# Kernel tuning notes

Measured on AMD Instinct MI355X. Metric: run time of the kernel, lower is better.

Reference implementation:

```python
import jax, jax.numpy as jnp
import numpy as np

B, T, VOCAB = 8192, 1024, 10000

def setup_inputs() -> dict:
    key = jax.random.key(0)
    k1, k2, k3, k4 = jax.random.split(key, 4)
    sample_seq = jax.random.randint(k1, (B, T), 0, VOCAB, dtype=jnp.int32)
    sample_seqLogprobs = jax.random.normal(k2, (B, T), dtype=jnp.float32)
    sample_value = jax.random.normal(k3, (B, T), dtype=jnp.float32)
    sample_reward = jax.random.normal(k4, (B, T), dtype=jnp.float32)
    return {
        "sample_seq": sample_seq,
        "sample_seqLogprobs": sample_seqLogprobs,
        "sample_value": sample_value,
        "sample_reward": sample_reward,
    }

def reference(sample_seq, sample_seqLogprobs, sample_value, sample_reward):
    # Vectorized version of the per-element python loop: zero out every token
    # at or after the first EOS (token id 0). cumsum>0 of the EOS indicator is
    # the running-max (cummax) of (seq==0).
    at_or_after_eos = jnp.cumsum((sample_seq == 0).astype(jnp.int32), axis=1) > 0
    seq = jnp.where(at_or_after_eos, 0, sample_seq)  # [B, T]

    # mask = (seq>0), shifted right by one with a leading column of ones
    mask = (seq > 0).astype(sample_seqLogprobs.dtype)
    mask = jnp.concatenate(
        [jnp.ones((mask.shape[0], 1), mask.dtype), mask[:, :-1]], axis=1
    )

    # sample_reward is a detached numpy array in the original (no grad)
    reward = jax.lax.stop_gradient(sample_reward)
    reward_diff = reward - sample_value  # [B, T]

    # masked REINFORCE loss, normalized by number of valid tokens
    output = -sample_seqLogprobs * reward_diff * mask
    loss = output.sum() / mask.sum()
    return loss
```

## Files before the change

### kernel.cpp

```cpp
#include <hip/hip_runtime.h>

#define BROWS 8192
#define TLEN  1024

__global__ __launch_bounds__(256) void row_reduce_kernel(
    const int*   __restrict__ seq,
    const float* __restrict__ logp,
    const float* __restrict__ value,
    const float* __restrict__ reward,
    double*      __restrict__ row_sum,
    double*      __restrict__ row_cnt)
{
    const int row  = blockIdx.x * 4 + (threadIdx.x >> 6);
    const int lane = threadIdx.x & 63;

    const size_t rowoff = (size_t)row * TLEN;
    const int4*   s4 = (const int4*)  (seq    + rowoff);
    const float4* l4 = (const float4*)(logp   + rowoff);
    const float4* v4 = (const float4*)(value  + rowoff);
    const float4* r4 = (const float4*)(reward + rowoff);

    int4   s[4];
    float4 l[4], v[4], r[4];
    #pragma unroll
    for (int k = 0; k < 4; ++k) {
        const int idx = k * 64 + lane;
        s[k] = s4[idx];
        l[k] = l4[idx];
        v[k] = v4[idx];
        r[k] = r4[idx];
    }

    int fz = TLEN;
    #pragma unroll
    for (int k = 3; k >= 0; --k) {
        const int base = k * 256 + lane * 4;
        if (s[k].w == 0) fz = base + 3;
        if (s[k].z == 0) fz = base + 2;
        if (s[k].y == 0) fz = base + 1;
        if (s[k].x == 0) fz = base + 0;
    }

    #pragma unroll
    for (int off = 32; off > 0; off >>= 1)
        fz = min(fz, __shfl_xor(fz, off, 64));

    double acc = 0.0;
    #pragma unroll
    for (int k = 0; k < 4; ++k) {
        const int base = k * 256 + lane * 4;
        if (base + 0 <= fz) acc += (double)(-l[k].x * (r[k].x - v[k].x));
        if (base + 1 <= fz) acc += (double)(-l[k].y * (r[k].y - v[k].y));
        if (base + 2 <= fz) acc += (double)(-l[k].z * (r[k].z - v[k].z));
        if (base + 3 <= fz) acc += (double)(-l[k].w * (r[k].w - v[k].w));
    }

    #pragma unroll
    for (int off = 32; off > 0; off >>= 1)
        acc += __shfl_xor(acc, off, 64);

    if (lane == 0) {
        row_sum[row] = acc;
        row_cnt[row] = (double)min(fz + 1, TLEN);
    }
}

__global__ __launch_bounds__(256) void final_reduce_kernel(
    const double* __restrict__ row_sum,
    const double* __restrict__ row_cnt,
    float*        __restrict__ out)
{
    const int tid  = threadIdx.x;
    const int lane = tid & 63;
    const int wave = tid >> 6;

    double s = 0.0, c = 0.0;
    for (int i = tid; i < BROWS; i += 256) {
        s += row_sum[i];
        c += row_cnt[i];
    }
    #pragma unroll
    for (int off = 32; off > 0; off >>= 1) {
        s += __shfl_xor(s, off, 64);
        c += __shfl_xor(c, off, 64);
    }
    __shared__ double ls[4], lc[4];
    if (lane == 0) { ls[wave] = s; lc[wave] = c; }
    __syncthreads();
    if (tid == 0) {
        double ts = ls[0] + ls[1] + ls[2] + ls[3];
        double tc = lc[0] + lc[1] + lc[2] + lc[3];
        out[0] = (float)(ts / tc);
    }
}

extern "C" void kernel_launch(void* const* d_in, const int* in_sizes, int n_in,
                              void* d_out, int out_size, void* d_ws, size_t ws_size,
                              hipStream_t stream) {
    const int*   seq    = (const int*)  d_in[0];
    const float* logp   = (const float*)d_in[1];
    const float* value  = (const float*)d_in[2];
    const float* reward = (const float*)d_in[3];
    float* out = (float*)d_out;

    double* row_sum = (double*)d_ws;
    double* row_cnt = row_sum + BROWS;

    row_reduce_kernel<<<BROWS / 4, 256, 0, stream>>>(seq, logp, value, reward,
                                                     row_sum, row_cnt);
    final_reduce_kernel<<<1, 256, 0, stream>>>(row_sum, row_cnt, out);
}
```

Baseline: 156.5 us.

## Split EOS-position scan and masked sum into separate kernels

The fused row kernel is split in two. The first kernel finds the first-EOS index per row and writes it out. The second kernel reads logprob, value and reward with one full row per 256-thread block, covering four strided rows, and sums per block; the final kernel derives the token count from the stored indices. This shrinks the per-row dependency so the float loads are not tied to the sequence scan, but it adds an extra kernel launch and serialises the two passes over memory.

Result: no change. 156.0 us (-0.3%).

```diff
diff --git a/kernel.cpp b/kernel.cpp
--- a/kernel.cpp
+++ b/kernel.cpp
@@ -2,34 +2,21 @@
 
 #define BROWS 8192
 #define TLEN  1024
+#define NBLK  2048
+#define RPB   4
 
-__global__ __launch_bounds__(256) void row_reduce_kernel(
-    const int*   __restrict__ seq,
-    const float* __restrict__ logp,
-    const float* __restrict__ value,
-    const float* __restrict__ reward,
-    double*      __restrict__ row_sum,
-    double*      __restrict__ row_cnt)
+__global__ __launch_bounds__(256) void fz_kernel(
+    const int* __restrict__ seq,
+    int*       __restrict__ fz_out)
 {
     const int row  = blockIdx.x * 4 + (threadIdx.x >> 6);
     const int lane = threadIdx.x & 63;
 
-    const size_t rowoff = (size_t)row * TLEN;
-    const int4*   s4 = (const int4*)  (seq    + rowoff);
-    const float4* l4 = (const float4*)(logp   + rowoff);
-    const float4* v4 = (const float4*)(value  + rowoff);
-    const float4* r4 = (const float4*)(reward + rowoff);
-
-    int4   s[4];
-    float4 l[4], v[4], r[4];
+    const int4* s4 = (const int4*)(seq + (size_t)row * TLEN);
+    int4 s[4];
     #pragma unroll
-    for (int k = 0; k < 4; ++k) {
-        const int idx = k * 64 + lane;
-        s[k] = s4[idx];
-        l[k] = l4[idx];
-        v[k] = v4[idx];
-        r[k] = r4[idx];
-    }
+    for (int k = 0; k < 4; ++k)
+        s[k] = s4[k * 64 + lane];
 
     int fz = TLEN;
     #pragma unroll
@@ -40,34 +27,58 @@
         if (s[k].y == 0) fz = base + 1;
         if (s[k].x == 0) fz = base + 0;
     }
-
     #pragma unroll
     for (int off = 32; off > 0; off >>= 1)
         fz = min(fz, __shfl_xor(fz, off, 64));
 
+    if (lane == 0) fz_out[row] = fz;
+}
+
+__global__ __launch_bounds__(256) void sum_kernel(
+    const float* __restrict__ logp,
+    const float* __restrict__ value,
+    const float* __restrict__ reward,
+    const int*   __restrict__ fz_in,
+    double*      __restrict__ blk_sum)
+{
+    const int tid = threadIdx.x;
+
+    float4 l[RPB], v[RPB], r[RPB];
+    int    fz[RPB];
+    #pragma unroll
+    for (int k = 0; k < RPB; ++k) {
+        const int    row = blockIdx.x + k * NBLK;
+        const size_t off = (size_t)row * TLEN;
+        l[k]  = ((const float4*)(logp   + off))[tid];
+        v[k]  = ((const float4*)(value  + off))[tid];
+        r[k]  = ((const float4*)(reward + off))[tid];
+        fz[k] = fz_in[row];
+    }
+
+    const int t0 = tid * 4;
     double acc = 0.0;
     #pragma unroll
-    for (int k = 0; k < 4; ++k) {
-        const int base = k * 256 + lane * 4;
-        if (base + 0 <= fz) acc += (double)(-l[k].x * (r[k].x - v[k].x));
-        if (base + 1 <= fz) acc += (double)(-l[k].y * (r[k].y - v[k].y));
-        if (base + 2 <= fz) acc += (double)(-l[k].z * (r[k].z - v[k].z));
-        if (base + 3 <= fz) acc += (double)(-l[k].w * (r[k].w - v[k].w));
+    for (int k = 0; k < RPB; ++k) {
+        if (t0 + 0 <= fz[k]) acc += (double)(-l[k].x * (r[k].x - v[k].x));
+        if (t0 + 1 <= fz[k]) acc += (double)(-l[k].y * (r[k].y - v[k].y));
+        if (t0 + 2 <= fz[k]) acc += (double)(-l[k].z * (r[k].z - v[k].z));
+        if (t0 + 3 <= fz[k]) acc += (double)(-l[k].w * (r[k].w - v[k].w));
     }
 
     #pragma unroll
     for (int off = 32; off > 0; off >>= 1)
         acc += __shfl_xor(acc, off, 64);
 
-    if (lane == 0) {
-        row_sum[row] = acc;
-        row_cnt[row] = (double)min(fz + 1, TLEN);
-    }
+    __shared__ double ls[4];
+    if ((tid & 63) == 0) ls[tid >> 6] = acc;
+    __syncthreads();
+    if (tid == 0)
+        blk_sum[blockIdx.x] = ls[0] + ls[1] + ls[2] + ls[3];
 }
 
-__global__ __launch_bounds__(256) void final_reduce_kernel(
-    const double* __restrict__ row_sum,
-    const double* __restrict__ row_cnt,
+__global__ __launch_bounds__(256) void final_kernel(
+    const double* __restrict__ blk_sum,
+    const int*    __restrict__ fz_in,
     float*        __restrict__ out)
 {
     const int tid  = threadIdx.x;
@@ -75,10 +86,11 @@
     const int wave = tid >> 6;
 
     double s = 0.0, c = 0.0;
-    for (int i = tid; i < BROWS; i += 256) {
-        s += row_sum[i];
-        c += row_cnt[i];
-    }
+    for (int i = tid; i < NBLK; i += 256)
+        s += blk_sum[i];
+    for (int i = tid; i < BROWS; i += 256)
+        c += (double)min(fz_in[i] + 1, TLEN);
+
     #pragma unroll
     for (int off = 32; off > 0; off >>= 1) {
         s += __shfl_xor(s, off, 64);
@@ -103,10 +115,10 @@
     const float* reward = (const float*)d_in[3];
     float* out = (float*)d_out;
 
-    double* row_sum = (double*)d_ws;
-    double* row_cnt = row_sum + BROWS;
+    int*    fz      = (int*)d_ws;
+    double* blk_sum = (double*)((char*)d_ws + 65536);
 
-    row_reduce_kernel<<<BROWS / 4, 256, 0, stream>>>(seq, logp, value, reward,
-                                                     row_sum, row_cnt);
-    final_reduce_kernel<<<1, 256, 0, stream>>>(row_sum, row_cnt, out);
+    fz_kernel   <<<BROWS / 4, 256, 0, stream>>>(seq, fz);
+    sum_kernel  <<<NBLK,      256, 0, stream>>>(logp, value, reward, fz, blk_sum);
+    final_kernel<<<1,         256, 0, stream>>>(blk_sum, fz, out);
 }
```
